# Performance work log

Hardware: AMD Instinct MI355X
Metric: run time of the kernel (lower is better)

Reference implementation:

```python
import jax, jax.numpy as jnp
import numpy as np

NUM_NODES = 100000
NUM_EDGES = 1600000
D = 128

def sage_conv(x, src, dst, Wl, bl, Wr):
    # PyG SAGEConv (mean aggr): out = lin_l(mean_{j->i} x_j) + lin_r(x_i)
    msgs = x[src]                                            # [E, D] gather
    agg = jax.ops.segment_sum(msgs, dst, num_segments=x.shape[0])  # [N, D]
    deg = jax.ops.segment_sum(jnp.ones((src.shape[0],), x.dtype), dst,
                              num_segments=x.shape[0])       # [N]
    mean = agg / jnp.maximum(deg, 1.0)[:, None]
    return mean @ Wl.T + bl + x @ Wr.T

def setup_inputs() -> dict:
    key = jax.random.key(0)
    ks = jax.random.split(key, 16)
    s = 1.0 / np.sqrt(D)
    inp = {
        'x': jax.random.randint(ks[0], (NUM_NODES, 1), 0, NUM_NODES),
        'edge_index': jax.random.randint(ks[1], (2, NUM_EDGES), 0, NUM_NODES),
        'batch': jnp.zeros((NUM_NODES,), dtype=jnp.int64),
        'item_emb': jax.random.normal(ks[2], (NUM_NODES, D), jnp.float32),
        'edge_emb': jax.random.normal(ks[3], (NUM_EDGES, D), jnp.float32),
        'Wl1': jax.random.uniform(ks[4], (D, D), jnp.float32, -s, s),
        'bl1': jnp.zeros((D,), jnp.float32),
        'Wr1': jax.random.uniform(ks[5], (D, D), jnp.float32, -s, s),
        'Wl2': jax.random.uniform(ks[6], (D, D), jnp.float32, -s, s),
        'bl2': jnp.zeros((D,), jnp.float32),
        'Wr2': jax.random.uniform(ks[7], (D, D), jnp.float32, -s, s),
        'Wl3': jax.random.uniform(ks[8], (D, D), jnp.float32, -s, s),
        'bl3': jnp.zeros((D,), jnp.float32),
        'Wr3': jax.random.uniform(ks[9], (D, D), jnp.float32, -s, s),
        'W_lin1': jax.random.uniform(ks[10], (D, D), jnp.float32, -s, s),
        'b_lin1': jnp.zeros((D,), jnp.float32),
        'W_lin2': jax.random.uniform(ks[11], (D, D), jnp.float32, -s, s),
        'b_lin2': jnp.zeros((D,), jnp.float32),
    }
    return inp

def reference(x, edge_index, batch, item_emb, edge_emb,
              Wl1, bl1, Wr1, Wl2, bl2, Wr2, Wl3, bl3, Wr3,
              W_lin1, b_lin1, W_lin2, b_lin2):
    src, dst = edge_index[0], edge_index[1]
    h = item_emb[x[:, 0]]                      # embedding lookup + squeeze(1) -> [N, D]
    e = edge_emb                               # edge_embedding(arange(E)) == full table
    h = jax.nn.relu(sage_conv(h, src, dst, Wl1, bl1, Wr1))
    h = jax.nn.relu(sage_conv(h, src, dst, Wl2, bl2, Wr2))
    h = jax.nn.relu(sage_conv(h, src, dst, Wl3, bl3, Wr3))
    h = jax.nn.relu(h @ W_lin1.T + b_lin1)     # dropout is identity in eval mode
    e_out = jax.nn.relu(e @ W_lin2.T + b_lin2)
    return h, e_out
```

## Files before the change

### kernel.cpp

```cpp
#include <hip/hip_runtime.h>

#define NN  100000
#define NNP 100096
#define NE  1600000
#define DD  128

typedef __attribute__((ext_vector_type(8))) short bf16x8;
typedef __attribute__((ext_vector_type(4))) float f32x4;

__device__ __forceinline__ float bf2f(unsigned short u){
  union { unsigned int i; float f; } v; v.i = ((unsigned int)u) << 16; return v.f;
}
__device__ __forceinline__ unsigned short f2bf(float f){
  union { float f; unsigned int i; } v; v.f = f;
  unsigned int u = v.i;
  return (unsigned short)((u + 0x7fffu + ((u >> 16) & 1u)) >> 16);
}
__device__ __forceinline__ unsigned int cvt_pk_bf16(float lo, float hi){
  unsigned int r;
  asm("v_cvt_pk_bf16_f32 %0, %1, %2" : "=v"(r) : "v"(lo), "v"(hi));
  return r;
}

struct WPtrs { const float* w[8]; };
__global__ __launch_bounds__(256) void cvt_w_all(WPtrs wp, unsigned short* __restrict__ o){
  int t = blockIdx.x * 256 + threadIdx.x;
  int m = t >> 13, i = t & 8191;
  float2 v = ((const float2*)wp.w[m])[i];
  ((unsigned int*)o)[t] = cvt_pk_bf16(v.x, v.y);
}

__device__ __forceinline__ void stage_mat(const unsigned short* __restrict__ Bg,
                                          unsigned short* sB){
  int t = threadIdx.x;
  #pragma unroll
  for (int it = 0; it < 8; ++it){
    int idx = it * 256 + t;
    int kc = idx >> 7, col = idx & 127;
    uint4 v = *(const uint4*)(Bg + (size_t)col * DD + kc * 8);
    *(uint4*)(sB + (size_t)idx * 8) = v;
  }
}

__device__ __forceinline__ void edge_run(const float* __restrict__ A,
    const unsigned short* __restrict__ Wg, const float* __restrict__ bias,
    float* __restrict__ out, unsigned short* sB, int tile0, int cnt)
{
  stage_mat(Wg, sB);
  __syncthreads();
  int wave = threadIdx.x >> 6, lane = threadIdx.x & 63;
  int lr = lane & 15, lk = lane >> 4;
  float bv[8];
  #pragma unroll
  for (int j = 0; j < 8; ++j) bv[j] = bias[j * 16 + lr];

  for (int t = 0; t < cnt; ++t){
    size_t r0 = (size_t)(tile0 + t) * 128 + (size_t)wave * 32;
    const float* Ap = A + (r0 + lr) * DD + lk * 8;
    bf16x8 a[2][4];
    #pragma unroll
    for (int g = 0; g < 2; ++g){
      #pragma unroll
      for (int ks = 0; ks < 4; ++ks){
        f32x4 a0 = *(const f32x4*)(Ap + (size_t)g * 16 * DD + ks * 32);
        f32x4 a1 = *(const f32x4*)(Ap + (size_t)g * 16 * DD + ks * 32 + 4);
        union { bf16x8 v; unsigned int u[4]; } au;
        au.u[0] = cvt_pk_bf16(a0[0], a0[1]);
        au.u[1] = cvt_pk_bf16(a0[2], a0[3]);
        au.u[2] = cvt_pk_bf16(a1[0], a1[1]);
        au.u[3] = cvt_pk_bf16(a1[2], a1[3]);
        a[g][ks] = au.v;
      }
    }
    f32x4 acc[2][8];
    #pragma unroll
    for (int g = 0; g < 2; ++g)
      #pragma unroll
      for (int j = 0; j < 8; ++j) acc[g][j] = (f32x4){0.f, 0.f, 0.f, 0.f};
    #pragma unroll
    for (int ks = 0; ks < 4; ++ks){
      #pragma unroll
      for (int j = 0; j < 8; ++j){
        bf16x8 b = *(const bf16x8*)(sB + ((ks * 4 + lk) * 128 + j * 16 + lr) * 8);
        acc[0][j] = __builtin_amdgcn_mfma_f32_16x16x32_bf16(a[0][ks], b, acc[0][j], 0, 0, 0);
        acc[1][j] = __builtin_amdgcn_mfma_f32_16x16x32_bf16(a[1][ks], b, acc[1][j], 0, 0, 0);
      }
    }
    #pragma unroll
    for (int g = 0; g < 2; ++g)
      #pragma unroll
      for (int j = 0; j < 8; ++j)
        #pragma unroll
        for (int r = 0; r < 4; ++r){
          size_t row = r0 + g * 16 + lk * 4 + r;
          out[row * DD + j * 16 + lr] = fmaxf(acc[g][j][r] + bv[j], 0.f);
        }
  }
}

#define EDGE_ARGS const float* __restrict__ eA, const unsigned short* __restrict__ eW, \
                  const float* __restrict__ eBias, float* __restrict__ eOut, \
                  int eTileBase, int eBlocks
#define EDGE_PASS eA, eW, eBias, eOut
#define EDGE_CHUNK 5

__global__ __launch_bounds__(256) void countdeg_edge(
    const int* __restrict__ dst, int* __restrict__ deg, int n, EDGE_ARGS){
  __shared__ unsigned short sB[16384];
  if ((int)blockIdx.x < eBlocks){
    edge_run(EDGE_PASS, sB, eTileBase + blockIdx.x * EDGE_CHUNK, EDGE_CHUNK);
    return;
  }
  int t = (blockIdx.x - eBlocks) * 256 + threadIdx.x;
  if (t < n) atomicAdd(&deg[dst[t]], 1);
}

__global__ __launch_bounds__(256) void fillcsr_edge(
    const int* __restrict__ src, const int* __restrict__ dst,
    const int* __restrict__ row_start, int* __restrict__ cursor,
    int* __restrict__ csr, int n, EDGE_ARGS){
  __shared__ unsigned short sB[16384];
  if ((int)blockIdx.x < eBlocks){
    edge_run(EDGE_PASS, sB, eTileBase + blockIdx.x * EDGE_CHUNK, EDGE_CHUNK);
    return;
  }
  int t = (blockIdx.x - eBlocks) * 256 + threadIdx.x;
  if (t < n){
    int d = dst[t];
    int pos = atomicAdd(&cursor[d], 1);
    csr[row_start[d] + pos] = src[t];
  }
}

#define SCAN_CHUNK 1024
__global__ __launch_bounds__(256) void partial_sums(const int* __restrict__ deg,
                                                    int* __restrict__ partials, int n){
  __shared__ int lds[256];
  int t = threadIdx.x;
  int base = blockIdx.x * SCAN_CHUNK + t * 4;
  int s = 0;
  #pragma unroll
  for (int i = 0; i < 4; ++i){ int idx = base + i; s += (idx < n) ? deg[idx] : 0; }
  lds[t] = s; __syncthreads();
  for (int off = 128; off > 0; off >>= 1){
    if (t < off) lds[t] += lds[t + off];
    __syncthreads();
  }
  if (t == 0) partials[blockIdx.x] = lds[0];
}

__global__ void scan_partials(int* partials, int nb){
  if (threadIdx.x == 0 && blockIdx.x == 0){
    int acc = 0;
    for (int i = 0; i < nb; ++i){ int v = partials[i]; partials[i] = acc; acc += v; }
  }
}

__global__ __launch_bounds__(256) void scan_block(const int* __restrict__ deg,
                                                  const int* __restrict__ partials,
                                                  int* __restrict__ row_start, int n){
  __shared__ int lds[256];
  int t = threadIdx.x;
  int base = blockIdx.x * SCAN_CHUNK + t * 4;
  int v[4]; int s = 0;
  #pragma unroll
  for (int i = 0; i < 4; ++i){ int idx = base + i; v[i] = (idx < n) ? deg[idx] : 0; s += v[i]; }
  lds[t] = s; __syncthreads();
  for (int off = 1; off < 256; off <<= 1){
    int x = (t >= off) ? lds[t - off] : 0;
    __syncthreads();
    lds[t] += x;
    __syncthreads();
  }
  int excl = ((t == 0) ? 0 : lds[t - 1]) + partials[blockIdx.x];
  #pragma unroll
  for (int i = 0; i < 4; ++i){ int idx = base + i; if (idx < n) row_start[idx] = excl; excl += v[i]; }
}

__global__ __launch_bounds__(256) void gather_h0(const int* __restrict__ x,
                                                 const float* __restrict__ emb,
                                                 unsigned short* __restrict__ h, int n){
  int t = blockIdx.x * 256 + threadIdx.x;
  if (t >= n * 64) return;
  int node = t >> 6, p = t & 63;
  int s = x[node];
  float2 v = *(const float2*)(emb + (size_t)s * DD + p * 2);
  ((unsigned int*)h)[t] = cvt_pk_bf16(v.x, v.y);
}

__global__ __launch_bounds__(256) void aggregate3(const unsigned short* __restrict__ h,
                                                  const int* __restrict__ csr,
                                                  const int* __restrict__ row_start,
                                                  const int* __restrict__ deg,
                                                  unsigned short* __restrict__ mean, int n){
  int node = blockIdx.x * 4 + (threadIdx.x >> 6);
  int lane = threadIdx.x & 63;
  int st = __builtin_amdgcn_readfirstlane(row_start[node]);
  int d  = __builtin_amdgcn_readfirstlane(deg[node]);
  const unsigned int* hp = (const unsigned int*)h;
  float a0[8], a1[8];
  #pragma unroll
  for (int k = 0; k < 8; ++k){ a0[k] = 0.f; a1[k] = 0.f; }
  int i = 0;
  for (; i + 8 <= d; i += 8){
    int idx[8];
    #pragma unroll
    for (int k = 0; k < 8; ++k) idx[k] = csr[st + i + k];
    unsigned int v[8];
    #pragma unroll
    for (int k = 0; k < 8; ++k) v[k] = hp[(size_t)idx[k] * 64 + lane];
    #pragma unroll
    for (int k = 0; k < 8; ++k){
      a0[k] += bf2f((unsigned short)(v[k] & 0xffffu));
      a1[k] += bf2f((unsigned short)(v[k] >> 16));
    }
  }
  for (; i + 4 <= d; i += 4){
    int idx[4];
    #pragma unroll
    for (int k = 0; k < 4; ++k) idx[k] = csr[st + i + k];
    unsigned int v[4];
    #pragma unroll
    for (int k = 0; k < 4; ++k) v[k] = hp[(size_t)idx[k] * 64 + lane];
    #pragma unroll
    for (int k = 0; k < 4; ++k){
      a0[k] += bf2f((unsigned short)(v[k] & 0xffffu));
      a1[k] += bf2f((unsigned short)(v[k] >> 16));
    }
  }
  for (; i < d; ++i){
    int s = csr[st + i];
    unsigned int v = hp[(size_t)s * 64 + lane];
    a0[0] += bf2f((unsigned short)(v & 0xffffu));
    a1[0] += bf2f((unsigned short)(v >> 16));
  }
  float s0 = ((a0[0] + a0[1]) + (a0[2] + a0[3])) + ((a0[4] + a0[5]) + (a0[6] + a0[7]));
  float s1 = ((a1[0] + a1[1]) + (a1[2] + a1[3])) + ((a1[4] + a1[5]) + (a1[6] + a1[7]));
  float inv = 1.0f / fmaxf((float)d, 1.0f);
  ((unsigned int*)mean)[(size_t)node * 64 + lane] = cvt_pk_bf16(s0 * inv, s1 * inv);
}

template<int DUAL, int OUTF32>
__global__ __launch_bounds__(256) void node_edge(
    const unsigned short* __restrict__ A1, const unsigned short* __restrict__ B1g,
    const unsigned short* __restrict__ A2, const unsigned short* __restrict__ B2g,
    const float* __restrict__ bias, void* __restrict__ outp, int M,
    EDGE_ARGS)
{
  __shared__ unsigned short sB[16384];
  if ((int)blockIdx.x < eBlocks){
    edge_run(EDGE_PASS, sB, eTileBase + blockIdx.x * EDGE_CHUNK, EDGE_CHUNK);
    return;
  }
  stage_mat(B1g, sB);
  int wave = threadIdx.x >> 6, lane = threadIdx.x & 63;
  int lr = lane & 15, lk = lane >> 4;
  float bv[8];
  #pragma unroll
  for (int j = 0; j < 8; ++j) bv[j] = bias[j * 16 + lr];

  int tile = blockIdx.x - eBlocks;
  size_t r0 = (size_t)tile * 128 + wave * 32;
  f32x4 acc[2][8];
  #pragma unroll
  for (int g = 0; g < 2; ++g)
    #pragma unroll
    for (int j = 0; j < 8; ++j) acc[g][j] = (f32x4){0.f, 0.f, 0.f, 0.f};

  bf16x8 a[2][4];
  {
    const unsigned short* Ap = A1 + (r0 + lr) * DD + lk * 8;
    #pragma unroll
    for (int g = 0; g < 2; ++g)
      #pragma unroll
      for (int ks = 0; ks < 4; ++ks)
        a[g][ks] = *(const bf16x8*)(Ap + (size_t)g * 16 * DD + ks * 32);
  }
  __syncthreads();
  #pragma unroll
  for (int ks = 0; ks < 4; ++ks){
    #pragma unroll
    for (int j = 0; j < 8; ++j){
      bf16x8 b = *(const bf16x8*)(sB + ((ks * 4 + lk) * 128 + j * 16 + lr) * 8);
      acc[0][j] = __builtin_amdgcn_mfma_f32_16x16x32_bf16(a[0][ks], b, acc[0][j], 0, 0, 0);
      acc[1][j] = __builtin_amdgcn_mfma_f32_16x16x32_bf16(a[1][ks], b, acc[1][j], 0, 0, 0);
    }
  }
  if (DUAL){
    __syncthreads();
    stage_mat(B2g, sB);
    {
      const unsigned short* Ap = A2 + (r0 + lr) * DD + lk * 8;
      #pragma unroll
      for (int g = 0; g < 2; ++g)
        #pragma unroll
        for (int ks = 0; ks < 4; ++ks)
          a[g][ks] = *(const bf16x8*)(Ap + (size_t)g * 16 * DD + ks * 32);
    }
    __syncthreads();
    #pragma unroll
    for (int ks = 0; ks < 4; ++ks){
      #pragma unroll
      for (int j = 0; j < 8; ++j){
        bf16x8 b = *(const bf16x8*)(sB + ((ks * 4 + lk) * 128 + j * 16 + lr) * 8);
        acc[0][j] = __builtin_amdgcn_mfma_f32_16x16x32_bf16(a[0][ks], b, acc[0][j], 0, 0, 0);
        acc[1][j] = __builtin_amdgcn_mfma_f32_16x16x32_bf16(a[1][ks], b, acc[1][j], 0, 0, 0);
      }
    }
  }
  #pragma unroll
  for (int g = 0; g < 2; ++g)
    #pragma unroll
    for (int j = 0; j < 8; ++j)
      #pragma unroll
      for (int r = 0; r < 4; ++r){
        size_t row = r0 + g * 16 + lk * 4 + r;
        float v = fmaxf(acc[g][j][r] + bv[j], 0.f);
        if (OUTF32){
          if (row < (size_t)M) ((float*)outp)[row * DD + j * 16 + lr] = v;
        } else {
          ((unsigned short*)outp)[row * DD + j * 16 + lr] = f2bf(v);
        }
      }
}

extern "C" void kernel_launch(void* const* d_in, const int* in_sizes, int n_in,
                              void* d_out, int out_size, void* d_ws, size_t ws_size,
                              hipStream_t stream)
{
  const int*   x    = (const int*)d_in[0];
  const int*   ei   = (const int*)d_in[1];
  const int*   srcp = ei;
  const int*   dstp = ei + NE;
  const float* item = (const float*)d_in[3];
  const float* eemb = (const float*)d_in[4];
  WPtrs wp;
  wp.w[0] = (const float*)d_in[5];
  wp.w[1] = (const float*)d_in[7];
  wp.w[2] = (const float*)d_in[8];
  wp.w[3] = (const float*)d_in[10];
  wp.w[4] = (const float*)d_in[11];
  wp.w[5] = (const float*)d_in[13];
  wp.w[6] = (const float*)d_in[14];
  wp.w[7] = (const float*)d_in[16];
  const float* bl1 = (const float*)d_in[6];
  const float* bl2 = (const float*)d_in[9];
  const float* bl3 = (const float*)d_in[12];
  const float* bq1 = (const float*)d_in[15];
  const float* bq2 = (const float*)d_in[17];

  char* ws = (char*)d_ws;
  size_t o = 0;
  auto alloc = [&](size_t bytes) -> void* {
    void* p = ws + o;
    o += (bytes + 255) & ~(size_t)255;
    return p;
  };
  unsigned short* wbf      = (unsigned short*)alloc(8 * 16384 * 2);
  int*            deg      = (int*)alloc((size_t)NNP * 4);
  int*            cursor   = (int*)alloc((size_t)NNP * 4);
  int*            row_st   = (int*)alloc((size_t)NNP * 4);
  int*            partials = (int*)alloc(4096);
  int*            csr      = (int*)alloc((size_t)NE * 4);
  unsigned short* mean     = (unsigned short*)alloc((size_t)NNP * DD * 2);
  unsigned short* h_a      = (unsigned short*)alloc((size_t)NNP * DD * 2);
  unsigned short* h_b      = (unsigned short*)alloc((size_t)NNP * DD * 2);

  float* out_h = (float*)d_out;
  float* out_e = out_h + (size_t)NN * DD;
  const unsigned short* eW = wbf + 7 * 16384;

  hipMemsetAsync(deg, 0, (size_t)NNP * 4 * 2, stream);

  cvt_w_all<<<256, 256, 0, stream>>>(wp, wbf);

  int eb = 0;
  const int e_cd = 250, e_fc = 250, e_nd = 500, e_fin = 500;

  const int nb = (NN + SCAN_CHUNK - 1) / SCAN_CHUNK;
  const int csr_blk = (NE + 255) / 256;

  countdeg_edge<<<e_cd + csr_blk, 256, 0, stream>>>(dstp, deg, NE,
      eemb, eW, bq2, out_e, eb * EDGE_CHUNK, e_cd); eb += e_cd;
  partial_sums<<<nb, 256, 0, stream>>>(deg, partials, NN);
  scan_partials<<<1, 64, 0, stream>>>(partials, nb);
  scan_block<<<nb, 256, 0, stream>>>(deg, partials, row_st, NN);
  fillcsr_edge<<<e_fc + csr_blk, 256, 0, stream>>>(srcp, dstp, row_st, cursor, csr, NE,
      eemb, eW, bq2, out_e, eb * EDGE_CHUNK, e_fc); eb += e_fc;

  gather_h0<<<(NN * 64 + 255) / 256, 256, 0, stream>>>(x, item, h_a, NN);

  const int agg_grid   = (NN + 3) / 4;
  const int node_tiles = NNP / 128;

  aggregate3<<<agg_grid, 256, 0, stream>>>(h_a, csr, row_st, deg, mean, NN);
  node_edge<1,0><<<e_nd + node_tiles, 256, 0, stream>>>(mean, wbf + 0*16384, h_a, wbf + 1*16384,
      bl1, h_b, NN, eemb, eW, bq2, out_e, eb * EDGE_CHUNK, e_nd); eb += e_nd;
  aggregate3<<<agg_grid, 256, 0, stream>>>(h_b, csr, row_st, deg, mean, NN);
  node_edge<1,0><<<e_nd + node_tiles, 256, 0, stream>>>(mean, wbf + 2*16384, h_b, wbf + 3*16384,
      bl2, h_a, NN, eemb, eW, bq2, out_e, eb * EDGE_CHUNK, e_nd); eb += e_nd;
  aggregate3<<<agg_grid, 256, 0, stream>>>(h_a, csr, row_st, deg, mean, NN);
  node_edge<1,0><<<e_nd + node_tiles, 256, 0, stream>>>(mean, wbf + 4*16384, h_a, wbf + 5*16384,
      bl3, h_b, NN, eemb, eW, bq2, out_e, eb * EDGE_CHUNK, e_nd); eb += e_nd;

  node_edge<0,1><<<e_fin + node_tiles, 256, 0, stream>>>(h_b, wbf + 6*16384, h_b, wbf + 6*16384,
      bq1, out_h, NN, eemb, eW, bq2, out_e, eb * EDGE_CHUNK, e_fin); eb += e_fin;
}
```

Baseline: 770.4 us.

## Overlap edge GEMM with scan kernels and widen aggregation loads to 8 bytes

```diff
diff --git a/kernel.cpp b/kernel.cpp
--- a/kernel.cpp
+++ b/kernel.cpp
@@ -133,11 +133,17 @@
 }
 
 #define SCAN_CHUNK 1024
-__global__ __launch_bounds__(256) void partial_sums(const int* __restrict__ deg,
-                                                    int* __restrict__ partials, int n){
-  __shared__ int lds[256];
+__global__ __launch_bounds__(256) void partials_edge(
+    const int* __restrict__ deg, int* __restrict__ partials, int n, EDGE_ARGS){
+  __shared__ unsigned short sB[16384];
+  if ((int)blockIdx.x < eBlocks){
+    edge_run(EDGE_PASS, sB, eTileBase + blockIdx.x * EDGE_CHUNK, EDGE_CHUNK);
+    return;
+  }
+  int* lds = (int*)sB;
+  int hb = blockIdx.x - eBlocks;
   int t = threadIdx.x;
-  int base = blockIdx.x * SCAN_CHUNK + t * 4;
+  int base = hb * SCAN_CHUNK + t * 4;
   int s = 0;
   #pragma unroll
   for (int i = 0; i < 4; ++i){ int idx = base + i; s += (idx < n) ? deg[idx] : 0; }
@@ -146,22 +152,48 @@
     if (t < off) lds[t] += lds[t + off];
     __syncthreads();
   }
-  if (t == 0) partials[blockIdx.x] = lds[0];
-}
-
-__global__ void scan_partials(int* partials, int nb){
-  if (threadIdx.x == 0 && blockIdx.x == 0){
-    int acc = 0;
-    for (int i = 0; i < nb; ++i){ int v = partials[i]; partials[i] = acc; acc += v; }
-  }
-}
-
-__global__ __launch_bounds__(256) void scan_block(const int* __restrict__ deg,
-                                                  const int* __restrict__ partials,
-                                                  int* __restrict__ row_start, int n){
-  __shared__ int lds[256];
+  if (t == 0) partials[hb] = lds[0];
+}
+
+__global__ __launch_bounds__(256) void scanp_edge(int* partials, int nb, EDGE_ARGS){
+  __shared__ unsigned short sB[16384];
+  if ((int)blockIdx.x >= 1){
+    int e = blockIdx.x - 1;
+    if (e < eBlocks) edge_run(EDGE_PASS, sB, eTileBase + e * EDGE_CHUNK, EDGE_CHUNK);
+    return;
+  }
+  if (threadIdx.x >= 64) return;
+  int lane = threadIdx.x;
+  int o0 = (lane < nb) ? partials[lane] : 0;
+  int o1 = (lane + 64 < nb) ? partials[lane + 64] : 0;
+  int v0 = o0, v1 = o1;
+  #pragma unroll
+  for (int off = 1; off < 64; off <<= 1){
+    int t = __shfl_up(v0, off, 64);
+    if (lane >= off) v0 += t;
+  }
+  int tot0 = __shfl(v0, 63, 64);
+  #pragma unroll
+  for (int off = 1; off < 64; off <<= 1){
+    int t = __shfl_up(v1, off, 64);
+    if (lane >= off) v1 += t;
+  }
+  if (lane < nb)      partials[lane]      = v0 - o0;
+  if (lane + 64 < nb) partials[lane + 64] = tot0 + v1 - o1;
+}
+
+__global__ __launch_bounds__(256) void scanb_edge(
+    const int* __restrict__ deg, const int* __restrict__ partials,
+    int* __restrict__ row_start, int n, EDGE_ARGS){
+  __shared__ unsigned short sB[16384];
+  if ((int)blockIdx.x < eBlocks){
+    edge_run(EDGE_PASS, sB, eTileBase + blockIdx.x * EDGE_CHUNK, EDGE_CHUNK);
+    return;
+  }
+  int* lds = (int*)sB;
+  int hb = blockIdx.x - eBlocks;
   int t = threadIdx.x;
-  int base = blockIdx.x * SCAN_CHUNK + t * 4;
+  int base = hb * SCAN_CHUNK + t * 4;
   int v[4]; int s = 0;
   #pragma unroll
   for (int i = 0; i < 4; ++i){ int idx = base + i; v[i] = (idx < n) ? deg[idx] : 0; s += v[i]; }
@@ -172,7 +204,7 @@
     lds[t] += x;
     __syncthreads();
   }
-  int excl = ((t == 0) ? 0 : lds[t - 1]) + partials[blockIdx.x];
+  int excl = ((t == 0) ? 0 : lds[t - 1]) + partials[hb];
   #pragma unroll
   for (int i = 0; i < 4; ++i){ int idx = base + i; if (idx < n) row_start[idx] = excl; excl += v[i]; }
 }
@@ -188,56 +220,56 @@
   ((unsigned int*)h)[t] = cvt_pk_bf16(v.x, v.y);
 }
 
-__global__ __launch_bounds__(256) void aggregate3(const unsigned short* __restrict__ h,
+__device__ __forceinline__ void add4(float* a, uint2 v){
+  a[0] += bf2f((unsigned short)(v.x & 0xffffu)); a[1] += bf2f((unsigned short)(v.x >> 16));
+  a[2] += bf2f((unsigned short)(v.y & 0xffffu)); a[3] += bf2f((unsigned short)(v.y >> 16));
+}
+
+__global__ __launch_bounds__(256) void aggregate4(const unsigned short* __restrict__ h,
                                                   const int* __restrict__ csr,
                                                   const int* __restrict__ row_start,
                                                   const int* __restrict__ deg,
                                                   unsigned short* __restrict__ mean, int n){
   int node = blockIdx.x * 4 + (threadIdx.x >> 6);
   int lane = threadIdx.x & 63;
+  int g = lane >> 5, c = lane & 31;
   int st = __builtin_amdgcn_readfirstlane(row_start[node]);
   int d  = __builtin_amdgcn_readfirstlane(deg[node]);
-  const unsigned int* hp = (const unsigned int*)h;
-  float a0[8], a1[8];
-  #pragma unroll
-  for (int k = 0; k < 8; ++k){ a0[k] = 0.f; a1[k] = 0.f; }
+  const uint2* hp2 = (const uint2*)h;
+  float acc[4] = {0.f, 0.f, 0.f, 0.f};
+
   int i = 0;
-  for (; i + 8 <= d; i += 8){
-    int idx[8];
-    #pragma unroll
-    for (int k = 0; k < 8; ++k) idx[k] = csr[st + i + k];
-    unsigned int v[8];
-    #pragma unroll
-    for (int k = 0; k < 8; ++k) v[k] = hp[(size_t)idx[k] * 64 + lane];
-    #pragma unroll
-    for (int k = 0; k < 8; ++k){
-      a0[k] += bf2f((unsigned short)(v[k] & 0xffffu));
-      a1[k] += bf2f((unsigned short)(v[k] >> 16));
-    }
+  for (; i + 16 <= d; i += 16){
+    int s[8];
+    #pragma unroll
+    for (int k = 0; k < 8; ++k) s[k] = csr[st + i + 2 * k + g];
+    uint2 v[8];
+    #pragma unroll
+    for (int k = 0; k < 8; ++k) v[k] = hp2[(size_t)s[k] * 32 + c];
+    #pragma unroll
+    for (int k = 0; k < 8; ++k) add4(acc, v[k]);
   }
   for (; i + 4 <= d; i += 4){
-    int idx[4];
-    #pragma unroll
-    for (int k = 0; k < 4; ++k) idx[k] = csr[st + i + k];
-    unsigned int v[4];
-    #pragma unroll
-    for (int k = 0; k < 4; ++k) v[k] = hp[(size_t)idx[k] * 64 + lane];
-    #pragma unroll
-    for (int k = 0; k < 4; ++k){
-      a0[k] += bf2f((unsigned short)(v[k] & 0xffffu));
-      a1[k] += bf2f((unsigned short)(v[k] >> 16));
-    }
-  }
-  for (; i < d; ++i){
-    int s = csr[st + i];
-    unsigned int v = hp[(size_t)s * 64 + lane];
-    a0[0] += bf2f((unsigned short)(v & 0xffffu));
-    a1[0] += bf2f((unsigned short)(v >> 16));
-  }
-  float s0 = ((a0[0] + a0[1]) + (a0[2] + a0[3])) + ((a0[4] + a0[5]) + (a0[6] + a0[7]));
-  float s1 = ((a1[0] + a1[1]) + (a1[2] + a1[3])) + ((a1[4] + a1[5]) + (a1[6] + a1[7]));
-  float inv = 1.0f / fmaxf((float)d, 1.0f);
-  ((unsigned int*)mean)[(size_t)node * 64 + lane] = cvt_pk_bf16(s0 * inv, s1 * inv);
+    int s0 = csr[st + i + g], s1 = csr[st + i + 2 + g];
+    uint2 v0 = hp2[(size_t)s0 * 32 + c];
+    uint2 v1 = hp2[(size_t)s1 * 32 + c];
+    add4(acc, v0); add4(acc, v1);
+  }
+  for (; i < d; i += 2){
+    int ii = i + g;
+    int s0 = csr[st + min(ii, d - 1)];
+    uint2 v0 = hp2[(size_t)s0 * 32 + c];
+    if (ii < d) add4(acc, v0);
+  }
+  #pragma unroll
+  for (int j = 0; j < 4; ++j) acc[j] += __shfl_xor(acc[j], 32, 64);
+  if (g == 0){
+    float inv = 1.0f / fmaxf((float)d, 1.0f);
+    uint2 o;
+    o.x = cvt_pk_bf16(acc[0] * inv, acc[1] * inv);
+    o.y = cvt_pk_bf16(acc[2] * inv, acc[3] * inv);
+    ((uint2*)mean)[(size_t)node * 32 + c] = o;
+  }
 }
 
 template<int DUAL, int OUTF32>
@@ -375,16 +407,20 @@
   cvt_w_all<<<256, 256, 0, stream>>>(wp, wbf);
 
   int eb = 0;
-  const int e_cd = 250, e_fc = 250, e_nd = 500, e_fin = 500;
+  const int e_cd = 250, e_ps = 100, e_sp = 100, e_sb = 100, e_fc = 250;
+  const int e_nd = 450, e_fin = 350;
 
   const int nb = (NN + SCAN_CHUNK - 1) / SCAN_CHUNK;
   const int csr_blk = (NE + 255) / 256;
 
   countdeg_edge<<<e_cd + csr_blk, 256, 0, stream>>>(dstp, deg, NE,
       eemb, eW, bq2, out_e, eb * EDGE_CHUNK, e_cd); eb += e_cd;
-  partial_sums<<<nb, 256, 0, stream>>>(deg, partials, NN);
-  scan_partials<<<1, 64, 0, stream>>>(partials, nb);
-  scan_block<<<nb, 256, 0, stream>>>(deg, partials, row_st, NN);
+  partials_edge<<<e_ps + nb, 256, 0, stream>>>(deg, partials, NN,
+      eemb, eW, bq2, out_e, eb * EDGE_CHUNK, e_ps); eb += e_ps;
+  scanp_edge<<<1 + e_sp, 256, 0, stream>>>(partials, nb,
+      eemb, eW, bq2, out_e, eb * EDGE_CHUNK, e_sp); eb += e_sp;
+  scanb_edge<<<e_sb + nb, 256, 0, stream>>>(deg, partials, row_st, NN,
+      eemb, eW, bq2, out_e, eb * EDGE_CHUNK, e_sb); eb += e_sb;
   fillcsr_edge<<<e_fc + csr_blk, 256, 0, stream>>>(srcp, dstp, row_st, cursor, csr, NE,
       eemb, eW, bq2, out_e, eb * EDGE_CHUNK, e_fc); eb += e_fc;
 
@@ -393,13 +429,13 @@
   const int agg_grid   = (NN + 3) / 4;
   const int node_tiles = NNP / 128;
 
-  aggregate3<<<agg_grid, 256, 0, stream>>>(h_a, csr, row_st, deg, mean, NN);
+  aggregate4<<<agg_grid, 256, 0, stream>>>(h_a, csr, row_st, deg, mean, NN);
   node_edge<1,0><<<e_nd + node_tiles, 256, 0, stream>>>(mean, wbf + 0*16384, h_a, wbf + 1*16384,
       bl1, h_b, NN, eemb, eW, bq2, out_e, eb * EDGE_CHUNK, e_nd); eb += e_nd;
-  aggregate3<<<agg_grid, 256, 0, stream>>>(h_b, csr, row_st, deg, mean, NN);
+  aggregate4<<<agg_grid, 256, 0, stream>>>(h_b, csr, row_st, deg, mean, NN);
   node_edge<1,0><<<e_nd + node_tiles, 256, 0, stream>>>(mean, wbf + 2*16384, h_b, wbf + 3*16384,
       bl2, h_a, NN, eemb, eW, bq2, out_e, eb * EDGE_CHUNK, e_nd); eb += e_nd;
-  aggregate3<<<agg_grid, 256, 0, stream>>>(h_a, csr, row_st, deg, mean, NN);
+  aggregate4<<<agg_grid, 256, 0, stream>>>(h_a, csr, row_st, deg, mean, NN);
   node_edge<1,0><<<e_nd + node_tiles, 256, 0, stream>>>(mean, wbf + 4*16384, h_a, wbf + 5*16384,
       bl3, h_b, NN, eemb, eW, bq2, out_e, eb * EDGE_CHUNK, e_nd); eb += e_nd;
 
```

Result: slower. 845.0 us (+9.7%).
